# Optimization experiments

Hardware: AMD Instinct MI355X
Metric: run time of the kernel (lower is better)

## Reference

```python
import jax, jax.numpy as jnp
import numpy as np

EMBED_DIM = 1024

def setup_inputs() -> dict:
    key = jax.random.key(0)
    ks = jax.random.split(key, 7)
    D = EMBED_DIM
    x = jax.random.normal(ks[0], (4, 2048, D), dtype=jnp.float32)
    s = 1.0 / np.sqrt(D)
    Wq = jax.random.normal(ks[1], (D, D), dtype=jnp.float32) * s
    bq = jnp.zeros((D,), dtype=jnp.float32)
    Wk = jax.random.normal(ks[2], (D, D), dtype=jnp.float32) * s
    bk = jnp.zeros((D,), dtype=jnp.float32)
    Wv = jax.random.normal(ks[3], (D, D), dtype=jnp.float32) * s
    bv = jnp.zeros((D,), dtype=jnp.float32)
    return {"x": x, "Wq": Wq, "bq": bq, "Wk": Wk, "bk": bk, "Wv": Wv, "bv": bv}

def reference(x, Wq, bq, Wk, bk, Wv, bv):
    # x: [B,S,D]; torch Linear: x @ W.T + b -> here W is stored as [D_in, D_out]
    Q = jnp.einsum('bsd,de->bse', x, Wq) + bq
    K = jnp.einsum('bsd,de->bse', x, Wk) + bk
    V = jnp.einsum('bsd,de->bse', x, Wv) + bv
    scale = 1.0 / jnp.sqrt(jnp.asarray(x.shape[-1], dtype=x.dtype))
    scores = jnp.einsum('bqd,bkd->bqk', Q, K) * scale  # [B,S,S]
    probs = jax.nn.softmax(scores, axis=-1)
    # dropout is identity in eval mode
    return jnp.einsum('bqk,bkd->bqd', probs, V)
```

## Files before the change

kernel.cpp:

```cpp
#include <hip/hip_runtime.h>
#include <hip/hip_bf16.h>
#include <hip/hip_fp16.h>
#include <stdint.h>
#include <stddef.h>
#include <string.h>

#define D_EMB 1024
#define SEQ   2048
#define BATCH 4

typedef short bf16x8  __attribute__((ext_vector_type(8)));
typedef short short8  __attribute__((ext_vector_type(8)));
typedef float f32x4   __attribute__((ext_vector_type(4)));

#define AS1 __attribute__((address_space(1)))
#define AS3 __attribute__((address_space(3)))

static __device__ __forceinline__ void async_copy16(const void* g, void* l) {
  __builtin_amdgcn_global_load_lds((const AS1 void*)g, (AS3 void*)l, 16, 0, 0);
}


#define BAR     __builtin_amdgcn_s_barrier()
#define VMCNT4  asm volatile("s_waitcnt vmcnt(4)" ::: "memory")
#define VMCNT0  asm volatile("s_waitcnt vmcnt(0)" ::: "memory")

#define STAGE_A(buf, h, kt) do {                                              \
    const __hip_bfloat16* _g = gA + (size_t)((h) * 128) * lda + ((kt) << 6);  \
    char* _l = (char*)sA + (buf) * 32768 + (h) * 16384 + wave * 1024;         \
    async_copy16(_g, _l);                                                     \
    async_copy16(_g + (size_t)64 * lda, _l + 8192);                           \
  } while (0)
#define STAGE_B(buf, h, kt) do {                                              \
    const __hip_bfloat16* _g = gB + (size_t)((h) * 128) * ldb + ((kt) << 6);  \
    char* _l = (char*)sB + (buf) * 32768 + (h) * 16384 + wave * 1024;         \
    async_copy16(_g, _l);                                                     \
    async_copy16(_g + (size_t)64 * ldb, _l + 8192);                           \
  } while (0)

#define LOAD_A(aF, lbuf, h) do {                                              \
    const __hip_bfloat16* _b = (lbuf) + (wr * 128 + (h) * 64 + lr) * 64;      \
    _Pragma("unroll")                                                         \
    for (int _i = 0; _i < 4; _i++) {                                          \
      aF[_i][0] = *(const bf16x8*)&_b[_i * 1024 + pc0];                       \
      aF[_i][1] = *(const bf16x8*)&_b[_i * 1024 + pc1];                       \
    }                                                                         \
  } while (0)
#define LOAD_B(bF, lbuf, g) do {                                              \
    const __hip_bfloat16* _b = (lbuf) + (wc * 64 + (g) * 32 + lr) * 64;       \
    _Pragma("unroll")                                                         \
    for (int _j = 0; _j < 2; _j++) {                                          \
      bF[_j][0] = *(const bf16x8*)&_b[_j * 1024 + pc0];                       \
      bF[_j][1] = *(const bf16x8*)&_b[_j * 1024 + pc1];                       \
    }                                                                         \
  } while (0)

#define MFMA_Q(aF, bF, h, g) do {                                             \
    __builtin_amdgcn_s_setprio(1);                                            \
    _Pragma("unroll")                                                         \
    for (int _i = 0; _i < 4; _i++)                                            \
      _Pragma("unroll")                                                       \
      for (int _j = 0; _j < 2; _j++) {                                        \
        acc[(h) * 4 + _i][(g) * 2 + _j] =                                     \
          __builtin_amdgcn_mfma_f32_16x16x32_bf16(aF[_i][0], bF[_j][0],       \
              acc[(h) * 4 + _i][(g) * 2 + _j], 0, 0, 0);                      \
        acc[(h) * 4 + _i][(g) * 2 + _j] =                                     \
          __builtin_amdgcn_mfma_f32_16x16x32_bf16(aF[_i][1], bF[_j][1],       \
              acc[(h) * 4 + _i][(g) * 2 + _j], 0, 0, 0);                      \
      }                                                                       \
    __builtin_amdgcn_s_setprio(0);                                            \
  } while (0)

static __device__ __forceinline__ void gemm256(
    const __hip_bfloat16* __restrict__ A, int lda,
    const __hip_bfloat16* __restrict__ Bt, int ldb,
    int K, f32x4 (&acc)[8][4])
{
  __shared__ __hip_bfloat16 sA[2][128 * 64 * 2];
  __shared__ __hip_bfloat16 sB[2][128 * 64 * 2];

  const int t    = threadIdx.x;
  const int wave = t >> 6;
  const int lane = t & 63;
  const int quad = lane >> 4;
  const int lr   = lane & 15;
  const int wr   = wave >> 2;
  const int wc   = wave & 3;

  const int r0 = t >> 3;
  const int cs = (((t & 7) ^ (r0 & 7)) << 3);
  const __hip_bfloat16* gA = A  + (size_t)r0 * lda + cs;
  const __hip_bfloat16* gB = Bt + (size_t)r0 * ldb + cs;

  const int pc0 = ((quad)     ^ (lr & 7)) << 3;
  const int pc1 = ((quad + 4) ^ (lr & 7)) << 3;

  const __hip_bfloat16* const lA0 = sA[0];
  const __hip_bfloat16* const lA1 = sA[1];
  const __hip_bfloat16* const lB0 = sB[0];
  const __hip_bfloat16* const lB1 = sB[1];

  const int nt    = K >> 6;
  const int niter = nt >> 1;

  STAGE_A(0, 0, 0);
  STAGE_A(0, 1, 0);
  STAGE_B(0, 0, 0);
  STAGE_B(0, 1, 0);
  STAGE_A(1, 0, 1);
  STAGE_B(1, 1, 1);
  VMCNT4;
  BAR;

  bf16x8 aF[4][2], bFa[2][2], bFb[2][2];

  for (int j = 0; j < niter - 1; ++j) {
    const int tb = 2 * j + 1, tc = tb + 1, td = tb + 2;

    LOAD_A(aF, lA0, 0); LOAD_B(bFa, lB0, 0);
    STAGE_B(1, 0, tb);
    BAR; MFMA_Q(aF, bFa, 0, 0); BAR;

    LOAD_B(bFb, lB0, 1);
    STAGE_A(1, 1, tb);
    BAR; MFMA_Q(aF, bFb, 0, 1); BAR;

    LOAD_A(aF, lA0, 1);
    STAGE_A(0, 0, tc);
    BAR; MFMA_Q(aF, bFb, 1, 1); BAR;

    STAGE_B(0, 1, tc);
    VMCNT4;
    BAR; MFMA_Q(aF, bFa, 1, 0); BAR;

    LOAD_A(aF, lA1, 0); LOAD_B(bFa, lB1, 0);
    STAGE_B(0, 0, tc);
    BAR; MFMA_Q(aF, bFa, 0, 0); BAR;

    LOAD_B(bFb, lB1, 1);
    STAGE_A(0, 1, tc);
    BAR; MFMA_Q(aF, bFb, 0, 1); BAR;

    LOAD_A(aF, lA1, 1);
    STAGE_A(1, 0, td);
    BAR; MFMA_Q(aF, bFb, 1, 1); BAR;

    STAGE_B(1, 1, td);
    VMCNT4;
    BAR; MFMA_Q(aF, bFa, 1, 0); BAR;
  }

  {
    const int tb = nt - 1;
    LOAD_A(aF, lA0, 0); LOAD_B(bFa, lB0, 0);
    STAGE_B(1, 0, tb);
    BAR; MFMA_Q(aF, bFa, 0, 0); BAR;

    LOAD_B(bFb, lB0, 1);
    STAGE_A(1, 1, tb);
    BAR; MFMA_Q(aF, bFb, 0, 1); BAR;

    LOAD_A(aF, lA0, 1);
    BAR; MFMA_Q(aF, bFb, 1, 1); BAR;

    VMCNT0;
    BAR; MFMA_Q(aF, bFa, 1, 0); BAR;

    LOAD_A(aF, lA1, 0); LOAD_B(bFa, lB1, 0);
    BAR; MFMA_Q(aF, bFa, 0, 0); BAR;

    LOAD_B(bFb, lB1, 1);
    BAR; MFMA_Q(aF, bFb, 0, 1); BAR;

    LOAD_A(aF, lA1, 1);
    BAR; MFMA_Q(aF, bFb, 1, 1); BAR;

    MFMA_Q(aF, bFa, 1, 0);
  }
}

#define ZERO_ACC(acc)                         \
  {                                           \
    f32x4 _z = {0.f, 0.f, 0.f, 0.f};          \
    _Pragma("unroll")                         \
    for (int _i = 0; _i < 8; _i++)            \
      _Pragma("unroll")                       \
      for (int _j = 0; _j < 4; _j++)          \
        acc[_i][_j] = _z;                     \
  }

__global__ __launch_bounds__(256) void prep_kernel(
    const float* __restrict__ x,
    const float* __restrict__ Wq,
    const float* __restrict__ Wk,
    const float* __restrict__ Wv,
    __hip_bfloat16* __restrict__ xb,
    __hip_bfloat16* __restrict__ Wt3)
{
  const int tx = threadIdx.x, ty = threadIdx.y;
  if (blockIdx.z == 3) {
    const int tid = ty * 32 + tx;
    const size_t base = ((size_t)blockIdx.y * 32 + blockIdx.x) * 8192;
#pragma unroll
    for (int p = 0; p < 8; p++) {
      const size_t i = base + p * 1024 + tid * 4;
      const float4 v = *(const float4*)(x + i);
      __hip_bfloat16 o[4] = {__float2bfloat16(v.x), __float2bfloat16(v.y),
                             __float2bfloat16(v.z), __float2bfloat16(v.w)};
      *(uint64_t*)(xb + i) = *(uint64_t*)o;
    }
    return;
  }
  const float* src = (blockIdx.z == 0) ? Wq : (blockIdx.z == 1) ? Wk : Wv;
  __hip_bfloat16* dst = Wt3 + (size_t)blockIdx.z * D_EMB * D_EMB;
  __shared__ __hip_bfloat16 tile[32][33];
  const int x0 = blockIdx.x * 32;
  const int y0 = blockIdx.y * 32;
#pragma unroll
  for (int i = 0; i < 32; i += 8)
    tile[ty + i][tx] = __float2bfloat16(src[(size_t)(y0 + ty + i) * D_EMB + (x0 + tx)]);
  __syncthreads();
#pragma unroll
  for (int i = 0; i < 32; i += 8)
    dst[(size_t)(x0 + ty + i) * D_EMB + (y0 + tx)] = tile[tx][ty + i];
}

__global__ __launch_bounds__(512, 2) void qkv_kernel(
    const __hip_bfloat16* __restrict__ xb,
    const __hip_bfloat16* __restrict__ Wt3,
    const float* __restrict__ bq,
    const float* __restrict__ bk,
    const float* __restrict__ bv,
    __hip_bfloat16* __restrict__ Q,
    __hip_bfloat16* __restrict__ Kb,
    __hip_bfloat16* __restrict__ Vt)
{
  const int mat = blockIdx.z;
  const int m0  = blockIdx.x * 256;
  const int n0  = blockIdx.y * 256;

  f32x4 acc[8][4];
  ZERO_ACC(acc);

  gemm256(xb + (size_t)m0 * D_EMB, D_EMB,
          Wt3 + (size_t)mat * D_EMB * D_EMB + (size_t)n0 * D_EMB, D_EMB,
          D_EMB, acc);

  const float* bias = (mat == 0) ? bq : (mat == 1) ? bk : bv;

  const int t = threadIdx.x;
  const int wave = t >> 6, lane = t & 63;
  const int quad = lane >> 4, lr = lane & 15;
  const int wr = wave >> 2, wc = wave & 3;

#pragma unroll
  for (int i = 0; i < 8; i++) {
#pragma unroll
    for (int j = 0; j < 4; j++) {
      const int n = n0 + wc * 64 + j * 16 + lr;
      const float bb = bias[n];
      const int mbase = m0 + wr * 128 + i * 16 + quad * 4;
      if (mat == 2) {
        const int b = mbase >> 11, s = mbase & 2047;
        __hip_bfloat16 pk[4];
#pragma unroll
        for (int r = 0; r < 4; r++) pk[r] = __float2bfloat16(acc[i][j][r] + bb);
        *(uint64_t*)&Vt[(size_t)b * D_EMB * SEQ + (size_t)n * SEQ + s] = *(uint64_t*)pk;
      } else {
        __hip_bfloat16* dst = (mat == 0) ? Q : Kb;
#pragma unroll
        for (int r = 0; r < 4; r++)
          dst[(size_t)(mbase + r) * D_EMB + n] = __float2bfloat16(acc[i][j][r] + bb);
      }
    }
  }
}

__global__ __launch_bounds__(512, 2) void scores_kernel(
    const __hip_bfloat16* __restrict__ Q,
    const __hip_bfloat16* __restrict__ Kb,
    __half* __restrict__ Sc)
{
  const int b  = blockIdx.z;
  const int m0 = blockIdx.y * 256;
  const int n0 = blockIdx.x * 256;

  f32x4 acc[8][4];
  ZERO_ACC(acc);

  gemm256(Q  + (size_t)b * SEQ * D_EMB + (size_t)m0 * D_EMB, D_EMB,
          Kb + (size_t)b * SEQ * D_EMB + (size_t)n0 * D_EMB, D_EMB,
          D_EMB, acc);

  __half* out = Sc + (size_t)b * SEQ * SEQ;
  const float scale = 0.03125f;

  const int t = threadIdx.x;
  const int wave = t >> 6, lane = t & 63;
  const int quad = lane >> 4, lr = lane & 15;
  const int wr = wave >> 2, wc = wave & 3;

#pragma unroll
  for (int i = 0; i < 8; i++)
#pragma unroll
    for (int j = 0; j < 4; j++) {
      const int n = n0 + wc * 64 + j * 16 + lr;
#pragma unroll
      for (int r = 0; r < 4; r++) {
        const int m = m0 + wr * 128 + i * 16 + quad * 4 + r;
        out[(size_t)m * SEQ + n] = __float2half(acc[i][j][r] * scale);
      }
    }
}

__global__ __launch_bounds__(256) void softmax_kernel(
    const __half* __restrict__ Sc, __hip_bfloat16* __restrict__ P)
{
  const int row = blockIdx.x;
  const __half* src = Sc + (size_t)row * SEQ;
  const int t = threadIdx.x;
  const int wave = t >> 6, lane = t & 63;

  const short8 raw = *(const short8*)(src + t * 8);
  float v[8];
#pragma unroll
  for (int i = 0; i < 8; i++) {
    const short si = raw[i];
    __half h;
    memcpy(&h, &si, sizeof(h));
    v[i] = __half2float(h);
  }

  float m = v[0];
#pragma unroll
  for (int i = 1; i < 8; i++) m = fmaxf(m, v[i]);
#pragma unroll
  for (int o = 32; o > 0; o >>= 1) m = fmaxf(m, __shfl_xor(m, o));

  __shared__ float redm[4];
  __shared__ float reds[4];
  if (lane == 0) redm[wave] = m;
  __syncthreads();
  m = fmaxf(fmaxf(redm[0], redm[1]), fmaxf(redm[2], redm[3]));

  float e[8], s = 0.f;
#pragma unroll
  for (int i = 0; i < 8; i++) { e[i] = __expf(v[i] - m); s += e[i]; }
#pragma unroll
  for (int o = 32; o > 0; o >>= 1) s += __shfl_xor(s, o);
  if (lane == 0) reds[wave] = s;
  __syncthreads();
  s = reds[0] + reds[1] + reds[2] + reds[3];

  const float inv = 1.f / s;
  short8 outp;
#pragma unroll
  for (int i = 0; i < 8; i++) {
    const __hip_bfloat16 b = __float2bfloat16(e[i] * inv);
    short sb;
    memcpy(&sb, &b, sizeof(sb));
    outp[i] = sb;
  }
  *(short8*)(P + (size_t)row * SEQ + t * 8) = outp;
}

__global__ __launch_bounds__(512, 2) void pv_kernel(
    const __hip_bfloat16* __restrict__ P,
    const __hip_bfloat16* __restrict__ Vt,
    float* __restrict__ out)
{
  const int b  = blockIdx.z;
  const int m0 = blockIdx.y * 256;
  const int n0 = blockIdx.x * 256;

  f32x4 acc[8][4];
  ZERO_ACC(acc);

  gemm256(P  + (size_t)b * SEQ * SEQ   + (size_t)m0 * SEQ, SEQ,
          Vt + (size_t)b * D_EMB * SEQ + (size_t)n0 * SEQ, SEQ,
          SEQ, acc);

  float* o = out + (size_t)b * SEQ * D_EMB;

  const int t = threadIdx.x;
  const int wave = t >> 6, lane = t & 63;
  const int quad = lane >> 4, lr = lane & 15;
  const int wr = wave >> 2, wc = wave & 3;

#pragma unroll
  for (int i = 0; i < 8; i++)
#pragma unroll
    for (int j = 0; j < 4; j++) {
      const int n = n0 + wc * 64 + j * 16 + lr;
#pragma unroll
      for (int r = 0; r < 4; r++) {
        const int m = m0 + wr * 128 + i * 16 + quad * 4 + r;
        o[(size_t)m * D_EMB + n] = acc[i][j][r];
      }
    }
}

extern "C" void kernel_launch(void* const* d_in, const int* in_sizes, int n_in,
                              void* d_out, int out_size, void* d_ws, size_t ws_size,
                              hipStream_t stream) {
  const float* x  = (const float*)d_in[0];
  const float* Wq = (const float*)d_in[1];
  const float* bq = (const float*)d_in[2];
  const float* Wk = (const float*)d_in[3];
  const float* bk = (const float*)d_in[4];
  const float* Wv = (const float*)d_in[5];
  const float* bv = (const float*)d_in[6];
  float* out = (float*)d_out;

  char* ws = (char*)d_ws;
  __hip_bfloat16* xb  = (__hip_bfloat16*)(ws);
  __hip_bfloat16* Wt3 = (__hip_bfloat16*)(ws + 16777216);
  __hip_bfloat16* Q   = (__hip_bfloat16*)(ws + 23068672);
  __hip_bfloat16* Kb  = (__hip_bfloat16*)(ws + 39845888);
  __hip_bfloat16* Vt  = (__hip_bfloat16*)(ws + 56623104);
  __half*         Sc  = (__half*)        (ws + 73400320);
  __hip_bfloat16* P   = (__hip_bfloat16*)(ws + 140509184);

  prep_kernel  <<<dim3(32, 32, 4), dim3(32, 8), 0, stream>>>(x, Wq, Wk, Wv, xb, Wt3);
  qkv_kernel   <<<dim3(32, 4, 3),  512,        0, stream>>>(xb, Wt3, bq, bk, bv, Q, Kb, Vt);
  scores_kernel<<<dim3(8, 8, 4),   512,        0, stream>>>(Q, Kb, Sc);
  softmax_kernel<<<dim3(8192),     256,        0, stream>>>(Sc, P);
  pv_kernel    <<<dim3(4, 8, 4),   512,        0, stream>>>(P, Vt, out);
}
```

Measured before the change: 270.9 us.

## Fuse softmax into PV GEMM with LDS-resident probabilities and deferred normalization

```diff
diff --git a/kernel.cpp b/kernel.cpp
--- a/kernel.cpp
+++ b/kernel.cpp
@@ -22,7 +22,7 @@
 
 
 #define BAR     __builtin_amdgcn_s_barrier()
-#define VMCNT4  asm volatile("s_waitcnt vmcnt(4)" ::: "memory")
+#define VMCNT6  asm volatile("s_waitcnt vmcnt(6)" ::: "memory")
 #define VMCNT0  asm volatile("s_waitcnt vmcnt(0)" ::: "memory")
 
 #define STAGE_A(buf, h, kt) do {                                              \
@@ -71,114 +71,6 @@
     __builtin_amdgcn_s_setprio(0);                                            \
   } while (0)
 
-static __device__ __forceinline__ void gemm256(
-    const __hip_bfloat16* __restrict__ A, int lda,
-    const __hip_bfloat16* __restrict__ Bt, int ldb,
-    int K, f32x4 (&acc)[8][4])
-{
-  __shared__ __hip_bfloat16 sA[2][128 * 64 * 2];
-  __shared__ __hip_bfloat16 sB[2][128 * 64 * 2];
-
-  const int t    = threadIdx.x;
-  const int wave = t >> 6;
-  const int lane = t & 63;
-  const int quad = lane >> 4;
-  const int lr   = lane & 15;
-  const int wr   = wave >> 2;
-  const int wc   = wave & 3;
-
-  const int r0 = t >> 3;
-  const int cs = (((t & 7) ^ (r0 & 7)) << 3);
-  const __hip_bfloat16* gA = A  + (size_t)r0 * lda + cs;
-  const __hip_bfloat16* gB = Bt + (size_t)r0 * ldb + cs;
-
-  const int pc0 = ((quad)     ^ (lr & 7)) << 3;
-  const int pc1 = ((quad + 4) ^ (lr & 7)) << 3;
-
-  const __hip_bfloat16* const lA0 = sA[0];
-  const __hip_bfloat16* const lA1 = sA[1];
-  const __hip_bfloat16* const lB0 = sB[0];
-  const __hip_bfloat16* const lB1 = sB[1];
-
-  const int nt    = K >> 6;
-  const int niter = nt >> 1;
-
-  STAGE_A(0, 0, 0);
-  STAGE_A(0, 1, 0);
-  STAGE_B(0, 0, 0);
-  STAGE_B(0, 1, 0);
-  STAGE_A(1, 0, 1);
-  STAGE_B(1, 1, 1);
-  VMCNT4;
-  BAR;
-
-  bf16x8 aF[4][2], bFa[2][2], bFb[2][2];
-
-  for (int j = 0; j < niter - 1; ++j) {
-    const int tb = 2 * j + 1, tc = tb + 1, td = tb + 2;
-
-    LOAD_A(aF, lA0, 0); LOAD_B(bFa, lB0, 0);
-    STAGE_B(1, 0, tb);
-    BAR; MFMA_Q(aF, bFa, 0, 0); BAR;
-
-    LOAD_B(bFb, lB0, 1);
-    STAGE_A(1, 1, tb);
-    BAR; MFMA_Q(aF, bFb, 0, 1); BAR;
-
-    LOAD_A(aF, lA0, 1);
-    STAGE_A(0, 0, tc);
-    BAR; MFMA_Q(aF, bFb, 1, 1); BAR;
-
-    STAGE_B(0, 1, tc);
-    VMCNT4;
-    BAR; MFMA_Q(aF, bFa, 1, 0); BAR;
-
-    LOAD_A(aF, lA1, 0); LOAD_B(bFa, lB1, 0);
-    STAGE_B(0, 0, tc);
-    BAR; MFMA_Q(aF, bFa, 0, 0); BAR;
-
-    LOAD_B(bFb, lB1, 1);
-    STAGE_A(0, 1, tc);
-    BAR; MFMA_Q(aF, bFb, 0, 1); BAR;
-
-    LOAD_A(aF, lA1, 1);
-    STAGE_A(1, 0, td);
-    BAR; MFMA_Q(aF, bFb, 1, 1); BAR;
-
-    STAGE_B(1, 1, td);
-    VMCNT4;
-    BAR; MFMA_Q(aF, bFa, 1, 0); BAR;
-  }
-
-  {
-    const int tb = nt - 1;
-    LOAD_A(aF, lA0, 0); LOAD_B(bFa, lB0, 0);
-    STAGE_B(1, 0, tb);
-    BAR; MFMA_Q(aF, bFa, 0, 0); BAR;
-
-    LOAD_B(bFb, lB0, 1);
-    STAGE_A(1, 1, tb);
-    BAR; MFMA_Q(aF, bFb, 0, 1); BAR;
-
-    LOAD_A(aF, lA0, 1);
-    BAR; MFMA_Q(aF, bFb, 1, 1); BAR;
-
-    VMCNT0;
-    BAR; MFMA_Q(aF, bFa, 1, 0); BAR;
-
-    LOAD_A(aF, lA1, 0); LOAD_B(bFa, lB1, 0);
-    BAR; MFMA_Q(aF, bFa, 0, 0); BAR;
-
-    LOAD_B(bFb, lB1, 1);
-    BAR; MFMA_Q(aF, bFb, 0, 1); BAR;
-
-    LOAD_A(aF, lA1, 1);
-    BAR; MFMA_Q(aF, bFb, 1, 1); BAR;
-
-    MFMA_Q(aF, bFa, 1, 0);
-  }
-}
-
 #define ZERO_ACC(acc)                         \
   {                                           \
     f32x4 _z = {0.f, 0.f, 0.f, 0.f};          \
@@ -188,6 +80,114 @@
       for (int _j = 0; _j < 4; _j++)          \
         acc[_i][_j] = _z;                     \
   }
+
+static __device__ __forceinline__ void gemm256(
+    const __hip_bfloat16* __restrict__ A, int lda,
+    const __hip_bfloat16* __restrict__ Bt, int ldb,
+    int K, f32x4 (&acc)[8][4])
+{
+  __shared__ __hip_bfloat16 sA[2][128 * 64 * 2];
+  __shared__ __hip_bfloat16 sB[2][128 * 64 * 2];
+
+  const int t    = threadIdx.x;
+  const int wave = t >> 6;
+  const int lane = t & 63;
+  const int quad = lane >> 4;
+  const int lr   = lane & 15;
+  const int wr   = wave >> 2;
+  const int wc   = wave & 3;
+
+  const int r0 = t >> 3;
+  const int cs = (((t & 7) ^ (r0 & 7)) << 3);
+  const __hip_bfloat16* gA = A  + (size_t)r0 * lda + cs;
+  const __hip_bfloat16* gB = Bt + (size_t)r0 * ldb + cs;
+
+  const int pc0 = ((quad)     ^ (lr & 7)) << 3;
+  const int pc1 = ((quad + 4) ^ (lr & 7)) << 3;
+
+  const __hip_bfloat16* const lA0 = sA[0];
+  const __hip_bfloat16* const lA1 = sA[1];
+  const __hip_bfloat16* const lB0 = sB[0];
+  const __hip_bfloat16* const lB1 = sB[1];
+
+  const int nt    = K >> 6;
+  const int niter = nt >> 1;
+
+  STAGE_A(0, 0, 0);
+  STAGE_A(0, 1, 0);
+  STAGE_B(0, 0, 0);
+  STAGE_B(0, 1, 0);
+  STAGE_B(1, 0, 1);
+  STAGE_B(1, 1, 1);
+  STAGE_A(1, 0, 1);
+  VMCNT6;
+  BAR;
+
+  bf16x8 aF[4][2], bFa[2][2], bFb[2][2];
+
+  for (int j = 0; j < niter - 1; ++j) {
+    const int tb = 2 * j + 1, tc = tb + 1, td = tb + 2;
+
+    LOAD_A(aF, lA0, 0); LOAD_B(bFa, lB0, 0);
+    STAGE_A(1, 1, tb);
+    BAR; MFMA_Q(aF, bFa, 0, 0); BAR;
+
+    LOAD_B(bFb, lB0, 1);
+    BAR; MFMA_Q(aF, bFb, 0, 1); BAR;
+
+    LOAD_A(aF, lA0, 1);
+    STAGE_B(0, 0, tc);
+    BAR; MFMA_Q(aF, bFb, 1, 1); BAR;
+
+    STAGE_B(0, 1, tc);
+    STAGE_A(0, 0, tc);
+    VMCNT6;
+    BAR; MFMA_Q(aF, bFa, 1, 0); BAR;
+
+    LOAD_A(aF, lA1, 0); LOAD_B(bFa, lB1, 0);
+    STAGE_A(0, 1, tc);
+    BAR; MFMA_Q(aF, bFa, 0, 0); BAR;
+
+    LOAD_B(bFb, lB1, 1);
+    BAR; MFMA_Q(aF, bFb, 0, 1); BAR;
+
+    LOAD_A(aF, lA1, 1);
+    STAGE_B(1, 0, td);
+    BAR; MFMA_Q(aF, bFb, 1, 1); BAR;
+
+    STAGE_B(1, 1, td);
+    STAGE_A(1, 0, td);
+    VMCNT6;
+    BAR; MFMA_Q(aF, bFa, 1, 0); BAR;
+  }
+
+  {
+    const int tb = nt - 1;
+    LOAD_A(aF, lA0, 0); LOAD_B(bFa, lB0, 0);
+    STAGE_A(1, 1, tb);
+    BAR; MFMA_Q(aF, bFa, 0, 0); BAR;
+
+    LOAD_B(bFb, lB0, 1);
+    BAR; MFMA_Q(aF, bFb, 0, 1); BAR;
+
+    LOAD_A(aF, lA0, 1);
+    BAR; MFMA_Q(aF, bFb, 1, 1); BAR;
+
+    VMCNT0;
+    BAR; MFMA_Q(aF, bFa, 1, 0); BAR;
+
+    LOAD_A(aF, lA1, 0); LOAD_B(bFa, lB1, 0);
+    BAR; MFMA_Q(aF, bFa, 0, 0); BAR;
+
+    LOAD_B(bFb, lB1, 1);
+    BAR; MFMA_Q(aF, bFb, 0, 1); BAR;
+
+    LOAD_A(aF, lA1, 1);
+    BAR; MFMA_Q(aF, bFb, 1, 1); BAR;
+
+    MFMA_Q(aF, bFa, 1, 0);
+  }
+}
 
 __global__ __launch_bounds__(256) void prep_kernel(
     const float* __restrict__ x,
@@ -313,91 +313,101 @@
     }
 }
 
-__global__ __launch_bounds__(256) void softmax_kernel(
-    const __half* __restrict__ Sc, __hip_bfloat16* __restrict__ P)
-{
-  const int row = blockIdx.x;
-  const __half* src = Sc + (size_t)row * SEQ;
-  const int t = threadIdx.x;
-  const int wave = t >> 6, lane = t & 63;
-
-  const short8 raw = *(const short8*)(src + t * 8);
-  float v[8];
-#pragma unroll
-  for (int i = 0; i < 8; i++) {
-    const short si = raw[i];
-    __half h;
-    memcpy(&h, &si, sizeof(h));
-    v[i] = __half2float(h);
-  }
-
-  float m = v[0];
-#pragma unroll
-  for (int i = 1; i < 8; i++) m = fmaxf(m, v[i]);
-#pragma unroll
-  for (int o = 32; o > 0; o >>= 1) m = fmaxf(m, __shfl_xor(m, o));
-
-  __shared__ float redm[4];
-  __shared__ float reds[4];
-  if (lane == 0) redm[wave] = m;
-  __syncthreads();
-  m = fmaxf(fmaxf(redm[0], redm[1]), fmaxf(redm[2], redm[3]));
-
-  float e[8], s = 0.f;
-#pragma unroll
-  for (int i = 0; i < 8; i++) { e[i] = __expf(v[i] - m); s += e[i]; }
-#pragma unroll
-  for (int o = 32; o > 0; o >>= 1) s += __shfl_xor(s, o);
-  if (lane == 0) reds[wave] = s;
-  __syncthreads();
-  s = reds[0] + reds[1] + reds[2] + reds[3];
-
-  const float inv = 1.f / s;
-  short8 outp;
-#pragma unroll
-  for (int i = 0; i < 8; i++) {
-    const __hip_bfloat16 b = __float2bfloat16(e[i] * inv);
-    short sb;
-    memcpy(&sb, &b, sizeof(sb));
-    outp[i] = sb;
-  }
-  *(short8*)(P + (size_t)row * SEQ + t * 8) = outp;
-}
-
-__global__ __launch_bounds__(512, 2) void pv_kernel(
-    const __hip_bfloat16* __restrict__ P,
+#define PROW 2056
+__global__ __launch_bounds__(512, 1) void smpv_kernel(
+    const __half* __restrict__ Sc,
     const __hip_bfloat16* __restrict__ Vt,
     float* __restrict__ out)
 {
+  __shared__ __hip_bfloat16 ldsP[32 * PROW];
+  __shared__ float linv[32];
+
   const int b  = blockIdx.z;
-  const int m0 = blockIdx.y * 256;
-  const int n0 = blockIdx.x * 256;
-
-  f32x4 acc[8][4];
-  ZERO_ACC(acc);
-
-  gemm256(P  + (size_t)b * SEQ * SEQ   + (size_t)m0 * SEQ, SEQ,
-          Vt + (size_t)b * D_EMB * SEQ + (size_t)n0 * SEQ, SEQ,
-          SEQ, acc);
-
-  float* o = out + (size_t)b * SEQ * D_EMB;
-
-  const int t = threadIdx.x;
+  const int m0 = blockIdx.x * 32;
+
+  const int t    = threadIdx.x;
+  const int row  = t >> 4;
+  const int col0 = (t & 15) * 16;
+
+  const __half* src = Sc + ((size_t)b * SEQ + (m0 + row)) * SEQ;
+
+  float vmax = -3.0e38f;
+#pragma unroll
+  for (int p = 0; p < 16; p++) {
+    const int off = (p >> 1) * 256 + (p & 1) * 8;
+    const short8 rv = *(const short8*)(src + col0 + off);
+#pragma unroll
+    for (int i = 0; i < 8; i++) {
+      __half h; const short sv = rv[i]; memcpy(&h, &sv, 2);
+      vmax = fmaxf(vmax, __half2float(h));
+    }
+  }
+#pragma unroll
+  for (int o = 1; o < 16; o <<= 1) vmax = fmaxf(vmax, __shfl_xor(vmax, o));
+
+  float lsum = 0.f;
+#pragma unroll
+  for (int p = 0; p < 16; p++) {
+    const int off = (p >> 1) * 256 + (p & 1) * 8;
+    const short8 rv = *(const short8*)(src + col0 + off);
+    short8 ov;
+#pragma unroll
+    for (int i = 0; i < 8; i++) {
+      __half h; const short sv = rv[i]; memcpy(&h, &sv, 2);
+      const float e = __expf(__half2float(h) - vmax);
+      lsum += e;
+      const __hip_bfloat16 eb = __float2bfloat16(e);
+      short so; memcpy(&so, &eb, 2);
+      ov[i] = so;
+    }
+    *(short8*)&ldsP[(size_t)row * PROW + col0 + off] = ov;
+  }
+#pragma unroll
+  for (int o = 1; o < 16; o <<= 1) lsum += __shfl_xor(lsum, o);
+  if ((t & 15) == 0) linv[row] = 1.f / lsum;
+  __syncthreads();
+
   const int wave = t >> 6, lane = t & 63;
   const int quad = lane >> 4, lr = lane & 15;
-  const int wr = wave >> 2, wc = wave & 3;
-
-#pragma unroll
-  for (int i = 0; i < 8; i++)
-#pragma unroll
-    for (int j = 0; j < 4; j++) {
-      const int n = n0 + wc * 64 + j * 16 + lr;
-#pragma unroll
-      for (int r = 0; r < 4; r++) {
-        const int m = m0 + wr * 128 + i * 16 + quad * 4 + r;
-        o[(size_t)m * D_EMB + n] = acc[i][j][r];
-      }
-    }
+  const int wr = wave >> 2;
+  const int wc = wave & 3;
+
+  f32x4 acc[16];
+  {
+    f32x4 z = {0.f, 0.f, 0.f, 0.f};
+#pragma unroll
+    for (int j = 0; j < 16; j++) acc[j] = z;
+  }
+
+  const __hip_bfloat16* aRow  = &ldsP[(size_t)(wr * 16 + lr) * PROW + quad * 8];
+  const __hip_bfloat16* bBase = Vt + (size_t)b * D_EMB * SEQ
+                                   + (size_t)(wc * 256 + lr) * SEQ + quad * 8;
+
+  for (int kc = 0; kc < 32; kc++) {
+    const int k0 = kc * 64;
+    const bf16x8 a0 = *(const bf16x8*)(aRow + k0);
+    const bf16x8 a1 = *(const bf16x8*)(aRow + k0 + 32);
+#pragma unroll
+    for (int j = 0; j < 16; j++) {
+      const bf16x8 b0 = *(const bf16x8*)(bBase + (size_t)j * 16 * SEQ + k0);
+      const bf16x8 b1 = *(const bf16x8*)(bBase + (size_t)j * 16 * SEQ + k0 + 32);
+      acc[j] = __builtin_amdgcn_mfma_f32_16x16x32_bf16(a0, b0, acc[j], 0, 0, 0);
+      acc[j] = __builtin_amdgcn_mfma_f32_16x16x32_bf16(a1, b1, acc[j], 0, 0, 0);
+    }
+  }
+
+  float il[4];
+#pragma unroll
+  for (int r = 0; r < 4; r++) il[r] = linv[wr * 16 + quad * 4 + r];
+
+  float* o = out + (size_t)b * SEQ * D_EMB;
+  const int orow = m0 + wr * 16 + quad * 4;
+  const int e0   = wc * 256 + lr;
+#pragma unroll
+  for (int j = 0; j < 16; j++)
+#pragma unroll
+    for (int r = 0; r < 4; r++)
+      o[(size_t)(orow + r) * D_EMB + e0 + j * 16] = acc[j][r] * il[r];
 }
 
 extern "C" void kernel_launch(void* const* d_in, const int* in_sizes, int n_in,
@@ -419,11 +429,9 @@
   __hip_bfloat16* Kb  = (__hip_bfloat16*)(ws + 39845888);
   __hip_bfloat16* Vt  = (__hip_bfloat16*)(ws + 56623104);
   __half*         Sc  = (__half*)        (ws + 73400320);
-  __hip_bfloat16* P   = (__hip_bfloat16*)(ws + 140509184);
 
   prep_kernel  <<<dim3(32, 32, 4), dim3(32, 8), 0, stream>>>(x, Wq, Wk, Wv, xb, Wt3);
   qkv_kernel   <<<dim3(32, 4, 3),  512,        0, stream>>>(xb, Wt3, bq, bk, bv, Q, Kb, Vt);
   scores_kernel<<<dim3(8, 8, 4),   512,        0, stream>>>(Q, Kb, Sc);
-  softmax_kernel<<<dim3(8192),     256,        0, stream>>>(Sc, P);
-  pv_kernel    <<<dim3(4, 8, 4),   512,        0, stream>>>(P, Vt, out);
-}
+  smpv_kernel  <<<dim3(64, 1, 4),  512,        0, stream>>>(Sc, Vt, out);
+}
```

Result: slower. 440.6 us (+62.6%).
